# Kernel optimization log

Measured on AMD Instinct MI355X. Metric: run time of the kernel, lower is better.

Reference implementation:

```python
import jax, jax.numpy as jnp
import numpy as np

IN_CH = 128
NUM_GROUPS = 32
EPS = 1e-5


def group_norm(x, weight, bias):
    b, c, h, w = x.shape
    g = NUM_GROUPS
    xg = x.reshape(b, g, c // g, h, w)
    mean = xg.mean(axis=(2, 3, 4), keepdims=True)
    var = xg.var(axis=(2, 3, 4), keepdims=True)
    xg = (xg - mean) * jax.lax.rsqrt(var + EPS)
    x = xg.reshape(b, c, h, w)
    return x * weight[None, :, None, None] + bias[None, :, None, None]


def conv1x1(x, w, b):
    # x: (b,c,h,w), w: (out,in), b: (out,)
    return jnp.einsum('oc,bchw->bohw', w, x) + b[None, :, None, None]


def setup_inputs() -> dict:
    key = jax.random.key(0)
    ks = jax.random.split(key, 6)
    b, c, h, w = 8, IN_CH, 64, 64
    scale = 1.0 / np.sqrt(c)  # xavier-ish scale for 1x1 convs
    return {
        'x': jax.random.normal(ks[0], (b, c, h, w), dtype=jnp.float32),
        'gn_weight': jnp.ones((c,), dtype=jnp.float32),
        'gn_bias': jnp.zeros((c,), dtype=jnp.float32),
        'wq': jax.random.normal(ks[1], (c, c), dtype=jnp.float32) * scale,
        'bq': jnp.zeros((c,), dtype=jnp.float32),
        'wk': jax.random.normal(ks[2], (c, c), dtype=jnp.float32) * scale,
        'bk': jnp.zeros((c,), dtype=jnp.float32),
        'wv': jax.random.normal(ks[3], (c, c), dtype=jnp.float32) * scale,
        'bv': jnp.zeros((c,), dtype=jnp.float32),
        'wo': jax.random.normal(ks[4], (c, c), dtype=jnp.float32) * scale,
        'bo': jnp.zeros((c,), dtype=jnp.float32),
        'gamma': jnp.ones((1,), dtype=jnp.float32),
    }


def reference(x, gn_weight, gn_bias, wq, bq, wk, bk, wv, bv, wo, bo, gamma):
    b, c, h, w = x.shape
    x_dash = group_norm(x, gn_weight, gn_bias)
    q = conv1x1(x_dash, wq, bq).reshape(b, c, h * w)  # (b,c,n)
    k = conv1x1(x_dash, wk, bk).reshape(b, c, h * w)
    v = conv1x1(x_dash, wv, bv).reshape(b, c, h * w)
    # attn[b,i,j] = sum_c q[b,c,i] k[b,c,j] / sqrt(c)
    attn = jnp.einsum('bci,bcj->bij', q, k) / jnp.sqrt(jnp.float32(c))
    attn = jax.nn.softmax(attn, axis=-1)
    # out[b,c,i] = sum_j v[b,c,j] attn[b,i,j]
    out = jnp.einsum('bcj,bij->bci', v, attn).reshape(b, c, h, w)
    out = conv1x1(out, wo, bo)
    return x + gamma[0] * out
```

## Files before the change

kernel.cpp:

```cpp
#include <hip/hip_runtime.h>

typedef unsigned short u16;
typedef unsigned int u32;
typedef __bf16 bf16_t;
typedef bf16_t bf16x8 __attribute__((ext_vector_type(8)));
typedef float f32x4 __attribute__((ext_vector_type(4)));
typedef u32 u32x4 __attribute__((ext_vector_type(4)));
typedef u32 u32x2 __attribute__((ext_vector_type(2)));

#define BATCH 8
#define CH 128
#define NSP 4096
#define LOG2E 1.44269504088896f

static __device__ __forceinline__ u16 f2bf(float f) {
  u32 u = __builtin_bit_cast(u32, f);
  u32 r = u + 0x7FFFu + ((u >> 16) & 1u);
  return (u16)(r >> 16);
}

static __device__ __forceinline__ bf16x8 ld_bf8(const u16* p) {
  return __builtin_bit_cast(bf16x8, *(const u32x4*)p);
}

static __device__ __forceinline__ f32x4 mfma16(bf16x8 a, bf16x8 b, f32x4 c) {
  return __builtin_amdgcn_mfma_f32_16x16x32_bf16(a, b, c, 0, 0, 0);
}

static __device__ __forceinline__ u32 cvt_pk(float lo, float hi) {
  u32 r;
  asm("v_cvt_pk_bf16_f32 %0, %1, %2" : "=v"(r) : "v"(lo), "v"(hi));
  return r;
}

static __device__ __forceinline__ float fast_exp2(float x) {
#if __has_builtin(__builtin_amdgcn_exp2f)
  return __builtin_amdgcn_exp2f(x);
#else
  return exp2f(x);
#endif
}

__global__ __launch_bounds__(256) void gn_stats_kernel(const float* __restrict__ x,
                                                       float* __restrict__ stats,
                                                       const float* __restrict__ wq,
                                                       const float* __restrict__ wk,
                                                       const float* __restrict__ wv,
                                                       const float* __restrict__ wo,
                                                       u16* __restrict__ wbf) {
  int bg = blockIdx.x;
  {
    int widx = bg * 256 + threadIdx.x;
    int m = widx >> 14, r = widx & 16383;
    const float* s = (m == 0) ? wq : (m == 1) ? wk : (m == 2) ? wv : wo;
    wbf[widx] = f2bf(s[r]);
  }
  const float4* p = (const float4*)(x + (size_t)bg * 16384);
  float s = 0.f, ss = 0.f;
  for (int i = threadIdx.x; i < 4096; i += 256) {
    float4 v = p[i];
    s += v.x + v.y + v.z + v.w;
    ss += v.x * v.x + v.y * v.y + v.z * v.z + v.w * v.w;
  }
  for (int off = 32; off; off >>= 1) {
    s += __shfl_xor(s, off);
    ss += __shfl_xor(ss, off);
  }
  __shared__ float rs[4], rss[4];
  int wave = threadIdx.x >> 6;
  if ((threadIdx.x & 63) == 0) { rs[wave] = s; rss[wave] = ss; }
  __syncthreads();
  if (threadIdx.x == 0) {
    s = rs[0] + rs[1] + rs[2] + rs[3];
    ss = rss[0] + rss[1] + rss[2] + rss[3];
    float mean = s * (1.f / 16384.f);
    float var = ss * (1.f / 16384.f) - mean * mean;
    stats[2 * bg] = mean;
    stats[2 * bg + 1] = rsqrtf(var + 1e-5f);
  }
}

__global__ __launch_bounds__(256) void qkv_kernel(const float* __restrict__ x,
                                                  const float* __restrict__ stats,
                                                  const float* __restrict__ gnw,
                                                  const float* __restrict__ gnb,
                                                  const u16* __restrict__ wqb,
                                                  const u16* __restrict__ wkb,
                                                  const u16* __restrict__ wvb,
                                                  const float* __restrict__ bq,
                                                  const float* __restrict__ bk,
                                                  const float* __restrict__ bv,
                                                  u16* __restrict__ q, u16* __restrict__ k,
                                                  u16* __restrict__ v) {
  __shared__ float tile[64][132];
  __shared__ float sc[128], sh[128];
  int b = blockIdx.y;
  int n0 = blockIdx.x * 64;
  int t = threadIdx.x;
  if (t < 128) {
    float mean = stats[2 * (b * 32 + (t >> 2))];
    float rstd = stats[2 * (b * 32 + (t >> 2)) + 1];
    float w = gnw[t];
    sc[t] = rstd * w;
    sh[t] = gnb[t] - mean * rstd * w;
  }
  __syncthreads();
  const float4* xb4 = (const float4*)(x + (size_t)b * CH * NSP);
#pragma unroll
  for (int i = 0; i < 8; ++i) {
    int idx = t + i * 256;
    int c = idx >> 4, j4 = idx & 15;
    float4 vv = xb4[(size_t)c * (NSP / 4) + (n0 >> 2) + j4];
    float s_ = sc[c], h_ = sh[c];
    tile[j4 * 4 + 0][c] = vv.x * s_ + h_;
    tile[j4 * 4 + 1][c] = vv.y * s_ + h_;
    tile[j4 * 4 + 2][c] = vv.z * s_ + h_;
    tile[j4 * 4 + 3][c] = vv.w * s_ + h_;
  }
  __syncthreads();

  int wave = t >> 6, lane = t & 63;
  int lr = lane & 15, lg = lane >> 4;
  int n_base = n0 + wave * 16;
  int row = wave * 16 + lr;

  bf16x8 xfr[4];
#pragma unroll
  for (int kk = 0; kk < 4; ++kk) {
    const float* p = &tile[row][kk * 32 + lg * 8];
    f32x4 lo = *(const f32x4*)p;
    f32x4 hi = *(const f32x4*)(p + 4);
    u32x4 xw = {cvt_pk(lo[0], lo[1]), cvt_pk(lo[2], lo[3]),
                cvt_pk(hi[0], hi[1]), cvt_pk(hi[2], hi[3])};
    xfr[kk] = __builtin_bit_cast(bf16x8, xw);
  }

  f32x4 accq[8] = {}, acck[8] = {}, accv[8] = {};
#pragma unroll
  for (int kk = 0; kk < 4; ++kk) {
    int coff = kk * 32 + lg * 8;
    bf16x8 xa = xfr[kk];
#pragma unroll
    for (int ot = 0; ot < 8; ++ot) {
      int woff = (ot * 16 + lr) * CH + coff;
      bf16x8 wqf = ld_bf8(wqb + woff);
      bf16x8 wkf = ld_bf8(wkb + woff);
      bf16x8 wvf = ld_bf8(wvb + woff);
      accq[ot] = mfma16(xa, wqf, accq[ot]);
      acck[ot] = mfma16(xa, wkf, acck[ot]);
      accv[ot] = mfma16(wvf, xa, accv[ot]);
    }
  }
  const float qscale = 0.08838834764831845f * LOG2E;
#pragma unroll
  for (int ot = 0; ot < 8; ++ot) {
    int o_col = ot * 16 + lr;
    float bqv = bq[o_col], bkv = bk[o_col];
#pragma unroll
    for (int r = 0; r < 4; ++r) {
      int nrow = n_base + lg * 4 + r;
      size_t off = ((size_t)b * NSP + nrow) * CH + o_col;
      q[off] = f2bf((accq[ot][r] + bqv) * qscale);
      k[off] = f2bf(acck[ot][r] + bkv);
    }
    int n_col = n_base + lr;
#pragma unroll
    for (int r = 0; r < 4; ++r) {
      int o_row = ot * 16 + lg * 4 + r;
      v[((size_t)b * CH + o_row) * NSP + n_col] = f2bf(accv[ot][r] + bv[o_row]);
    }
  }
}

#define KSTRIDE 136
#define VSTRIDE 72
__global__ __launch_bounds__(256, 2) void attn_kernel(const u16* __restrict__ q,
                                                      const u16* __restrict__ k,
                                                      const u16* __restrict__ v,
                                                      u16* __restrict__ part0,
                                                      u16* __restrict__ part1,
                                                      float* __restrict__ lbuf) {
  __shared__ __align__(16) u16 kbuf[2][64 * KSTRIDE];
  __shared__ __align__(16) u16 vbuf[2][128 * VSTRIDE];
  int id = blockIdx.x;
  int b = id & 7;
  int qblk = (id >> 3) & 31;
  int split = id >> 8;
  int wave = threadIdx.x >> 6, lane = threadIdx.x & 63;
  int lr = lane & 15, lg = lane >> 4;
  int i_base = qblk * 128 + wave * 32;
  int t0 = split * 32, t1 = t0 + 32;

  const u16* kg = k + (size_t)b * NSP * CH;
  const u16* vg = v + (size_t)b * CH * NSP;

  bf16x8 qa[2][4];
#pragma unroll
  for (int qt = 0; qt < 2; ++qt) {
    const u16* qrow = q + ((size_t)b * NSP + i_base + qt * 16 + lr) * CH;
#pragma unroll
    for (int kk = 0; kk < 4; ++kk) qa[qt][kk] = ld_bf8(qrow + kk * 32 + lg * 8);
  }

  int kgo[4], klo[4];
#pragma unroll
  for (int m = 0; m < 4; ++m) {
    int kr = wave * 16 + m * 4 + (lane >> 4);
    kgo[m] = kr * CH + (lane & 15) * 8;
    klo[m] = kr * KSTRIDE + (lane & 15) * 8;
  }
  int vgo[4][2], vlo[4];
  {
    int f = lane & 7;
    int p = ((lane >> 2) & 1) * 8 + (lane & 3);
#pragma unroll
    for (int w = 0; w < 4; ++w) {
      int c = wave * 32 + w * 8 + (lane >> 3);
      vgo[w][0] = c * NSP + p * 4;
      vgo[w][1] = c * NSP + (p + 4) * 4;
      vlo[w] = c * VSTRIDE + f * 8;
    }
  }

  u32x4 kstg[4];
  u32x2 vstg[4][2];
  auto KLOAD = [&](int t) {
    const u16* kt = kg + (size_t)t * (64 * CH);
#pragma unroll
    for (int m = 0; m < 4; ++m) kstg[m] = *(const u32x4*)(kt + kgo[m]);
  };
  auto VLOAD = [&](int t) {
    const u16* vt = vg + t * 64;
#pragma unroll
    for (int w = 0; w < 4; ++w) {
      vstg[w][0] = *(const u32x2*)(vt + vgo[w][0]);
      vstg[w][1] = *(const u32x2*)(vt + vgo[w][1]);
    }
  };
  auto KVWRITE = [&](int bi) {
    u16* kb2 = kbuf[bi];
    u16* vb2 = vbuf[bi];
#pragma unroll
    for (int m = 0; m < 4; ++m) *(u32x4*)(kb2 + klo[m]) = kstg[m];
#pragma unroll
    for (int w = 0; w < 4; ++w) {
      u32x4 d = {vstg[w][0][0], vstg[w][0][1], vstg[w][1][0], vstg[w][1][1]};
      *(u32x4*)(vb2 + vlo[w]) = d;
    }
  };

  KLOAD(t0);
  VLOAD(t0);
  asm volatile("s_waitcnt vmcnt(0)" ::: "memory");
  KVWRITE(0);
  KLOAD(t0 + 1);
  VLOAD(t0 + 1);
  asm volatile("s_waitcnt lgkmcnt(0)" ::: "memory");
  __builtin_amdgcn_s_barrier();
  __builtin_amdgcn_sched_barrier(0);

  f32x4 oacc[2][8] = {};
  float lsum[2] = {0.f, 0.f};

  for (int t = t0; t < t1; ++t) {
    int cur = (t - t0) & 1;
    const u16* kb = kbuf[cur];
    const u16* vb = vbuf[cur];

    f32x4 s[2][4] = {};
    __builtin_amdgcn_s_setprio(1);
#pragma unroll
    for (int kk = 0; kk < 4; ++kk) {
#pragma unroll
      for (int jt = 0; jt < 4; ++jt) {
        int row = jt * 16 + lr;
        bf16x8 kf = ld_bf8(kb + row * KSTRIDE + (kk * 4 + lg) * 8);
        s[0][jt] = mfma16(kf, qa[0][kk], s[0][jt]);
        s[1][jt] = mfma16(kf, qa[1][kk], s[1][jt]);
      }
    }
    __builtin_amdgcn_s_setprio(0);

#pragma unroll
    for (int kk2 = 0; kk2 < 2; ++kk2) {
      u32x4 paw[2];
#pragma unroll
      for (int qt = 0; qt < 2; ++qt) {
        float p0 = fast_exp2(s[qt][2 * kk2][0]);
        float p1 = fast_exp2(s[qt][2 * kk2][1]);
        float p2 = fast_exp2(s[qt][2 * kk2][2]);
        float p3 = fast_exp2(s[qt][2 * kk2][3]);
        float p4 = fast_exp2(s[qt][2 * kk2 + 1][0]);
        float p5 = fast_exp2(s[qt][2 * kk2 + 1][1]);
        float p6 = fast_exp2(s[qt][2 * kk2 + 1][2]);
        float p7 = fast_exp2(s[qt][2 * kk2 + 1][3]);
        lsum[qt] += ((p0 + p1) + (p2 + p3)) + ((p4 + p5) + (p6 + p7));
        paw[qt][0] = cvt_pk(p0, p1);
        paw[qt][1] = cvt_pk(p2, p3);
        paw[qt][2] = cvt_pk(p4, p5);
        paw[qt][3] = cvt_pk(p6, p7);
      }
      bf16x8 pa0 = __builtin_bit_cast(bf16x8, paw[0]);
      bf16x8 pa1 = __builtin_bit_cast(bf16x8, paw[1]);
      __builtin_amdgcn_s_setprio(1);
#pragma unroll
      for (int ct = 0; ct < 8; ++ct) {
        int c = ct * 16 + lr;
        bf16x8 vf = ld_bf8(vb + c * VSTRIDE + (kk2 * 4 + lg) * 8);
        oacc[0][ct] = mfma16(pa0, vf, oacc[0][ct]);
        oacc[1][ct] = mfma16(pa1, vf, oacc[1][ct]);
      }
      __builtin_amdgcn_s_setprio(0);
    }

    if (t + 1 < t1) {
      asm volatile("s_waitcnt vmcnt(0)" ::: "memory");
      KVWRITE(cur ^ 1);
      if (t + 2 < t1) {
        KLOAD(t + 2);
        VLOAD(t + 2);
      }
      asm volatile("s_waitcnt lgkmcnt(0)" ::: "memory");
      __builtin_amdgcn_s_barrier();
      __builtin_amdgcn_sched_barrier(0);
    }
  }

  u16* pdst = (split == 0) ? part0 : part1;
  float* ldst = lbuf + (size_t)split * (BATCH * NSP) + (size_t)b * NSP;
#pragma unroll
  for (int qt = 0; qt < 2; ++qt) {
    lsum[qt] += __shfl_xor(lsum[qt], 16);
    lsum[qt] += __shfl_xor(lsum[qt], 32);
    if (lg == 0) ldst[i_base + qt * 16 + lr] = lsum[qt];
#pragma unroll
    for (int r = 0; r < 4; ++r) {
      int i = i_base + qt * 16 + lg * 4 + r;
      u16* row = pdst + ((size_t)b * NSP + i) * CH;
#pragma unroll
      for (int ct = 0; ct < 8; ++ct) row[ct * 16 + lr] = f2bf(oacc[qt][ct][r]);
    }
  }
}

__global__ __launch_bounds__(256) void proj_kernel(const u16* __restrict__ p0,
                                                   const u16* __restrict__ p1,
                                                   const float* __restrict__ lbuf,
                                                   const u16* __restrict__ wob,
                                                   const float* __restrict__ bo,
                                                   const float* __restrict__ gamma,
                                                   const float* __restrict__ x,
                                                   float* __restrict__ out) {
  int b = blockIdx.y;
  int wave = threadIdx.x >> 6, lane = threadIdx.x & 63;
  int lr = lane & 15, lg = lane >> 4;
  int n_base = blockIdx.x * 64 + wave * 16;
  int nrow = n_base + lr;
  float linv = 1.f / (lbuf[(size_t)b * NSP + nrow] +
                      lbuf[(size_t)BATCH * NSP + (size_t)b * NSP + nrow]);
  const u16* r0 = p0 + ((size_t)b * NSP + nrow) * CH;
  const u16* r1 = p1 + ((size_t)b * NSP + nrow) * CH;
  f32x4 acc[8] = {};
#pragma unroll
  for (int kk = 0; kk < 4; ++kk) {
    int coff = kk * 32 + lg * 8;
    bf16x8 a = ld_bf8(r0 + coff);
    bf16x8 bb = ld_bf8(r1 + coff);
    u32 w0 = cvt_pk(((float)a[0] + (float)bb[0]) * linv, ((float)a[1] + (float)bb[1]) * linv);
    u32 w1 = cvt_pk(((float)a[2] + (float)bb[2]) * linv, ((float)a[3] + (float)bb[3]) * linv);
    u32 w2 = cvt_pk(((float)a[4] + (float)bb[4]) * linv, ((float)a[5] + (float)bb[5]) * linv);
    u32 w3 = cvt_pk(((float)a[6] + (float)bb[6]) * linv, ((float)a[7] + (float)bb[7]) * linv);
    u32x4 wv = {w0, w1, w2, w3};
    bf16x8 ofrag = __builtin_bit_cast(bf16x8, wv);
#pragma unroll
    for (int ot = 0; ot < 8; ++ot) {
      bf16x8 wf = ld_bf8(wob + (ot * 16 + lr) * CH + coff);
      acc[ot] = mfma16(wf, ofrag, acc[ot]);
    }
  }
  float g = gamma[0];
  int n_col = n_base + lr;
#pragma unroll
  for (int ot = 0; ot < 8; ++ot) {
#pragma unroll
    for (int r = 0; r < 4; ++r) {
      int o_row = ot * 16 + lg * 4 + r;
      size_t off = ((size_t)b * CH + o_row) * NSP + n_col;
      out[off] = x[off] + g * (acc[ot][r] + bo[o_row]);
    }
  }
}

extern "C" void kernel_launch(void* const* d_in, const int* in_sizes, int n_in,
                              void* d_out, int out_size, void* d_ws, size_t ws_size,
                              hipStream_t stream) {
  const float* x = (const float*)d_in[0];
  const float* gnw = (const float*)d_in[1];
  const float* gnb = (const float*)d_in[2];
  const float* wq = (const float*)d_in[3];
  const float* bq = (const float*)d_in[4];
  const float* wk = (const float*)d_in[5];
  const float* bk = (const float*)d_in[6];
  const float* wv = (const float*)d_in[7];
  const float* bv = (const float*)d_in[8];
  const float* wo = (const float*)d_in[9];
  const float* bo = (const float*)d_in[10];
  const float* gamma = (const float*)d_in[11];
  float* out = (float*)d_out;

  const size_t BUF = (size_t)BATCH * NSP * CH * sizeof(u16);
  char* ws = (char*)d_ws;
  u16* wbf = (u16*)ws;
  float* stats = (float*)(ws + 131072);
  u16* xd = (u16*)(ws + 262144);
  u16* qb = (u16*)(ws + 262144 + BUF);
  u16* kb = (u16*)(ws + 262144 + 2 * BUF);
  u16* vb = (u16*)(ws + 262144 + 3 * BUF);
  float* lbuf = (float*)(ws + 262144 + 4 * BUF);
  const size_t need = 262144 + 4 * BUF + 262144;
  if (ws_size < need) return;
  u16* part1 = (ws_size >= need + BUF) ? (u16*)(ws + need) : qb;

  gn_stats_kernel<<<256, 256, 0, stream>>>(x, stats, wq, wk, wv, wo, wbf);
  qkv_kernel<<<dim3(64, 8), 256, 0, stream>>>(x, stats, gnw, gnb, wbf, wbf + 16384,
                                              wbf + 32768, bq, bk, bv, qb, kb, vb);
  attn_kernel<<<512, 256, 0, stream>>>(qb, kb, vb, xd, part1, lbuf);
  proj_kernel<<<dim3(64, 8), 256, 0, stream>>>(xd, part1, lbuf, wbf + 49152, bo, gamma,
                                               x, out);
}
```

Measured before the change: 135.6 us.

## Stage K/V tiles with direct global-to-LDS loads and pre-swizzled layouts

The attention kernel now copies K and V tiles straight into LDS with global_load_lds instead of routing them through registers and separate LDS writes. To make that possible without padded strides, the QKV projection kernel writes K and V to global memory in an XOR-swizzled order, so LDS reads stay free of bank conflicts on unpadded tiles. V is also stored with a permuted column order inside each 64-column block so the staged tile already matches the PV MFMA fragment layout. This frees staging registers and VALU work but relies on every K/V writer and reader agreeing on the permutation, and the per-iteration wait-then-barrier now sits at the top of the loop.

```diff
diff --git a/kernel.cpp b/kernel.cpp
--- a/kernel.cpp
+++ b/kernel.cpp
@@ -6,7 +6,6 @@
 typedef bf16_t bf16x8 __attribute__((ext_vector_type(8)));
 typedef float f32x4 __attribute__((ext_vector_type(4)));
 typedef u32 u32x4 __attribute__((ext_vector_type(4)));
-typedef u32 u32x2 __attribute__((ext_vector_type(2)));
 
 #define BATCH 8
 #define CH 128
@@ -39,6 +38,11 @@
 #else
   return exp2f(x);
 #endif
+}
+
+static __device__ __forceinline__ void gl2lds16(const u16* g, u16* l) {
+  __builtin_amdgcn_global_load_lds((const __attribute__((address_space(1))) void*)g,
+                                   (__attribute__((address_space(3))) void*)l, 16, 0, 0);
 }
 
 __global__ __launch_bounds__(256) void gn_stats_kernel(const float* __restrict__ x,
@@ -152,6 +156,9 @@
     }
   }
   const float qscale = 0.08838834764831845f * LOG2E;
+  int jj = wave * 16 + lr;
+  int frv = (jj >> 5) * 4 + ((jj & 15) >> 2);
+  int ev = (lr & 3) + ((wave & 1) << 2);
 #pragma unroll
   for (int ot = 0; ot < 8; ++ot) {
     int o_col = ot * 16 + lr;
@@ -159,29 +166,28 @@
 #pragma unroll
     for (int r = 0; r < 4; ++r) {
       int nrow = n_base + lg * 4 + r;
-      size_t off = ((size_t)b * NSP + nrow) * CH + o_col;
-      q[off] = f2bf((accq[ot][r] + bqv) * qscale);
-      k[off] = f2bf(acck[ot][r] + bkv);
-    }
-    int n_col = n_base + lr;
+      q[((size_t)b * NSP + nrow) * CH + o_col] = f2bf((accq[ot][r] + bqv) * qscale);
+      int cperm = ((((o_col >> 3) ^ (nrow & 7)) << 3)) | (o_col & 7);
+      k[((size_t)b * NSP + nrow) * CH + cperm] = f2bf(acck[ot][r] + bkv);
+    }
 #pragma unroll
     for (int r = 0; r < 4; ++r) {
-      int o_row = ot * 16 + lg * 4 + r;
-      v[((size_t)b * CH + o_row) * NSP + n_col] = f2bf(accv[ot][r] + bv[o_row]);
-    }
-  }
-}
-
-#define KSTRIDE 136
-#define VSTRIDE 72
+      int c = ot * 16 + lg * 4 + r;
+      int slot = frv ^ (c & 7);
+      v[((size_t)(b * CH + c)) * NSP + blockIdx.x * 64 + slot * 8 + ev] =
+          f2bf(accv[ot][r] + bv[c]);
+    }
+  }
+}
+
 __global__ __launch_bounds__(256, 2) void attn_kernel(const u16* __restrict__ q,
                                                       const u16* __restrict__ k,
                                                       const u16* __restrict__ v,
                                                       u16* __restrict__ part0,
                                                       u16* __restrict__ part1,
                                                       float* __restrict__ lbuf) {
-  __shared__ __align__(16) u16 kbuf[2][64 * KSTRIDE];
-  __shared__ __align__(16) u16 vbuf[2][128 * VSTRIDE];
+  __shared__ __align__(16) u16 kbuf[2][64 * 128];
+  __shared__ __align__(16) u16 vbuf[2][128 * 64];
   int id = blockIdx.x;
   int b = id & 7;
   int qblk = (id >> 3) & 31;
@@ -202,62 +208,22 @@
     for (int kk = 0; kk < 4; ++kk) qa[qt][kk] = ld_bf8(qrow + kk * 32 + lg * 8);
   }
 
-  int kgo[4], klo[4];
-#pragma unroll
-  for (int m = 0; m < 4; ++m) {
-    int kr = wave * 16 + m * 4 + (lane >> 4);
-    kgo[m] = kr * CH + (lane & 15) * 8;
-    klo[m] = kr * KSTRIDE + (lane & 15) * 8;
-  }
-  int vgo[4][2], vlo[4];
-  {
-    int f = lane & 7;
-    int p = ((lane >> 2) & 1) * 8 + (lane & 3);
-#pragma unroll
-    for (int w = 0; w < 4; ++w) {
-      int c = wave * 32 + w * 8 + (lane >> 3);
-      vgo[w][0] = c * NSP + p * 4;
-      vgo[w][1] = c * NSP + (p + 4) * 4;
-      vlo[w] = c * VSTRIDE + f * 8;
-    }
-  }
-
-  u32x4 kstg[4];
-  u32x2 vstg[4][2];
-  auto KLOAD = [&](int t) {
-    const u16* kt = kg + (size_t)t * (64 * CH);
-#pragma unroll
-    for (int m = 0; m < 4; ++m) kstg[m] = *(const u32x4*)(kt + kgo[m]);
+  auto STAGEK = [&](int t, int bi) {
+    const u16* src = kg + ((size_t)(t * 64 + wave * 16)) * CH + lane * 8;
+    u16* dst = &kbuf[bi][wave * 16 * 128];
+#pragma unroll
+    for (int g = 0; g < 4; ++g) gl2lds16(src + g * 512, dst + g * 512);
   };
-  auto VLOAD = [&](int t) {
-    const u16* vt = vg + t * 64;
-#pragma unroll
-    for (int w = 0; w < 4; ++w) {
-      vstg[w][0] = *(const u32x2*)(vt + vgo[w][0]);
-      vstg[w][1] = *(const u32x2*)(vt + vgo[w][1]);
-    }
+  int vco = wave * 32 + (lane >> 3);
+  auto STAGEV = [&](int t, int bi) {
+    const u16* src = vg + t * 64 + (lane & 7) * 8;
+    u16* dst = &vbuf[bi][wave * 32 * 64];
+#pragma unroll
+    for (int g = 0; g < 4; ++g) gl2lds16(src + (size_t)(vco + g * 8) * NSP, dst + g * 512);
   };
-  auto KVWRITE = [&](int bi) {
-    u16* kb2 = kbuf[bi];
-    u16* vb2 = vbuf[bi];
-#pragma unroll
-    for (int m = 0; m < 4; ++m) *(u32x4*)(kb2 + klo[m]) = kstg[m];
-#pragma unroll
-    for (int w = 0; w < 4; ++w) {
-      u32x4 d = {vstg[w][0][0], vstg[w][0][1], vstg[w][1][0], vstg[w][1][1]};
-      *(u32x4*)(vb2 + vlo[w]) = d;
-    }
-  };
-
-  KLOAD(t0);
-  VLOAD(t0);
-  asm volatile("s_waitcnt vmcnt(0)" ::: "memory");
-  KVWRITE(0);
-  KLOAD(t0 + 1);
-  VLOAD(t0 + 1);
-  asm volatile("s_waitcnt lgkmcnt(0)" ::: "memory");
-  __builtin_amdgcn_s_barrier();
-  __builtin_amdgcn_sched_barrier(0);
+
+  STAGEK(t0, 0);
+  STAGEV(t0, 0);
 
   f32x4 oacc[2][8] = {};
   float lsum[2] = {0.f, 0.f};
@@ -266,6 +232,14 @@
     int cur = (t - t0) & 1;
     const u16* kb = kbuf[cur];
     const u16* vb = vbuf[cur];
+    asm volatile("s_waitcnt vmcnt(0)" ::: "memory");
+    __builtin_amdgcn_s_barrier();
+    __builtin_amdgcn_sched_barrier(0);
+    if (t + 1 < t1) {
+      STAGEK(t + 1, cur ^ 1);
+      STAGEV(t + 1, cur ^ 1);
+    }
+    __builtin_amdgcn_sched_barrier(0);
 
     f32x4 s[2][4] = {};
     __builtin_amdgcn_s_setprio(1);
@@ -274,7 +248,7 @@
 #pragma unroll
       for (int jt = 0; jt < 4; ++jt) {
         int row = jt * 16 + lr;
-        bf16x8 kf = ld_bf8(kb + row * KSTRIDE + (kk * 4 + lg) * 8);
+        bf16x8 kf = ld_bf8(kb + row * 128 + ((((kk << 2) + lg) ^ (row & 7)) << 3));
         s[0][jt] = mfma16(kf, qa[0][kk], s[0][jt]);
         s[1][jt] = mfma16(kf, qa[1][kk], s[1][jt]);
       }
@@ -306,23 +280,11 @@
 #pragma unroll
       for (int ct = 0; ct < 8; ++ct) {
         int c = ct * 16 + lr;
-        bf16x8 vf = ld_bf8(vb + c * VSTRIDE + (kk2 * 4 + lg) * 8);
+        bf16x8 vf = ld_bf8(vb + c * 64 + ((((kk2 << 2) + lg) ^ (c & 7)) << 3));
         oacc[0][ct] = mfma16(pa0, vf, oacc[0][ct]);
         oacc[1][ct] = mfma16(pa1, vf, oacc[1][ct]);
       }
       __builtin_amdgcn_s_setprio(0);
-    }
-
-    if (t + 1 < t1) {
-      asm volatile("s_waitcnt vmcnt(0)" ::: "memory");
-      KVWRITE(cur ^ 1);
-      if (t + 2 < t1) {
-        KLOAD(t + 2);
-        VLOAD(t + 2);
-      }
-      asm volatile("s_waitcnt lgkmcnt(0)" ::: "memory");
-      __builtin_amdgcn_s_barrier();
-      __builtin_amdgcn_sched_barrier(0);
     }
   }
 
```

Result: faster. 127.4 us (-6.1%).
